# Kernel tuning notes

Hardware: AMD Instinct MI355X
Metric: run time of the kernel (lower is better)

The kernel has to match this reference:

```python
import jax, jax.numpy as jnp
import numpy as np

EMBED_DIM = 1024
NUM_HEADS = 16
HEAD_DIM = EMBED_DIM // NUM_HEADS
MAX_DIST = 128
NUM_BUCKETS = 2 * MAX_DIST + 1  # 257: fixes off-by-one in original Embedding sizing


def setup_inputs() -> dict:
    key = jax.random.key(0)
    ks = jax.random.split(key, 10)
    B, S, D = 2, 2048, EMBED_DIM
    s = 1.0 / np.sqrt(D)
    return {
        "x": jax.random.normal(ks[0], (B, S, D), dtype=jnp.float32),
        "Wq": jax.random.normal(ks[1], (D, D), dtype=jnp.float32) * s,
        "bq": jnp.zeros((D,), dtype=jnp.float32),
        "Wk": jax.random.normal(ks[2], (D, D), dtype=jnp.float32) * s,
        "bk": jnp.zeros((D,), dtype=jnp.float32),
        "Wv": jax.random.normal(ks[3], (D, D), dtype=jnp.float32) * s,
        "bv": jnp.zeros((D,), dtype=jnp.float32),
        "Wo": jax.random.normal(ks[4], (D, D), dtype=jnp.float32) * s,
        "bo": jnp.zeros((D,), dtype=jnp.float32),
        "rel_emb": jax.random.normal(ks[5], (NUM_BUCKETS, NUM_HEADS), dtype=jnp.float32) * 0.02,
    }


def _rel_bias(rel_emb, seq_len):
    # relative position clamped to [-MAX_DIST, MAX_DIST], shifted to [0, 2*MAX_DIST]
    pos = jnp.arange(seq_len)
    rel = jnp.clip(pos[:, None] - pos[None, :], -MAX_DIST, MAX_DIST) + MAX_DIST
    bias = rel_emb[rel]                    # [S, S, H]
    return jnp.transpose(bias, (2, 0, 1))  # [H, S, S]


def reference(x, Wq, bq, Wk, bk, Wv, bv, Wo, bo, rel_emb):
    B, S, D = x.shape
    H, Hd = NUM_HEADS, HEAD_DIM
    # torch Linear: y = x @ W.T + b
    q = (x @ Wq.T + bq).reshape(B, S, H, Hd).transpose(0, 2, 1, 3)  # [B,H,S,Hd]
    k = (x @ Wk.T + bk).reshape(B, S, H, Hd).transpose(0, 2, 1, 3)
    v = (x @ Wv.T + bv).reshape(B, S, H, Hd).transpose(0, 2, 1, 3)
    scores = jnp.einsum("bhqd,bhkd->bhqk", q, k) / jnp.sqrt(jnp.float32(Hd))
    scores = scores + _rel_bias(rel_emb, S)[None]  # add [H,S,S] bias
    probs = jax.nn.softmax(scores, axis=-1)
    out = jnp.einsum("bhqk,bhkd->bhqd", probs, v)
    out = out.transpose(0, 2, 1, 3).reshape(B, S, D)
    return out @ Wo.T + bo
```

## Files before the change

### kernel.cpp

```cpp
#include <hip/hip_runtime.h>
#include <hip/hip_bf16.h>
#include <cstdint>
#include <cstddef>

#define DEVI __device__ __forceinline__

static constexpr int SEQ = 2048;
static constexpr int DM  = 1024;
static constexpr int NH  = 16;
static constexpr int HD  = 64;
static constexpr int NTOK = 2 * SEQ;
static constexpr int NBUCKET = 257;
static constexpr float LOG2E = 1.44269504088896f;

typedef __attribute__((ext_vector_type(8))) short bf16x8;
typedef __attribute__((ext_vector_type(4))) float f32x4;
typedef __attribute__((ext_vector_type(16))) float f32x16;
typedef __attribute__((ext_vector_type(2))) unsigned int uint32x2;
#define MFMA16(a, b, c) __builtin_amdgcn_mfma_f32_16x16x32_bf16((a), (b), (c), 0, 0, 0)
#define MFMA32(a, b, c) __builtin_amdgcn_mfma_f32_32x32x16_bf16((a), (b), (c), 0, 0, 0)

DEVI float bf1(uint16_t u)  { return __uint_as_float(((uint32_t)u) << 16); }
DEVI uint16_t f2bf(float f) {
    uint32_t x = __float_as_uint(f);
    x += 0x7fffu + ((x >> 16) & 1u);
    return (uint16_t)(x >> 16);
}
DEVI bf16x8 ld_frag(const uint16_t* p) {
    union { uint4 u; bf16x8 f; } c;
    c.u = *(const uint4*)p;
    return c.f;
}
DEVI void gld16(const uint16_t* g, uint16_t* l) {
    __builtin_amdgcn_global_load_lds(
        (const __attribute__((address_space(1))) uint32_t*)g,
        (__attribute__((address_space(3))) uint32_t*)l, 16, 0, 0);
}
DEVI uint32_t cvt_pk_bf16(float lo, float hi) {
    uint32_t r;
    asm("v_cvt_pk_bf16_f32 %0, %1, %2" : "=v"(r) : "v"(lo), "v"(hi));
    return r;
}
DEVI void pl32(uint32_t &a, uint32_t &b) {
    const uint32x2 r = __builtin_amdgcn_permlane32_swap(a, b, false, false);
    a = r[0]; b = r[1];
}

__global__ void sniff_kernel(const uint16_t* __restrict__ x, int* __restrict__ flag)
{
    int bad = 0;
    for (int i = threadIdx.x; i < 512; i += 64) {
        const float v = bf1(x[i]);
        if (!(fabsf(v) < 64.0f)) bad = 1;
    }
    const unsigned long long m = __ballot(bad);
    if (threadIdx.x == 0) *flag = (m != 0ull) ? 1 : 0;
}

__global__ __launch_bounds__(256)
void convert_kernel(const void* __restrict__ x, const void* __restrict__ Wq,
                    const void* __restrict__ Wk, const void* __restrict__ Wv,
                    const void* __restrict__ Wo, const void* __restrict__ bq,
                    const void* __restrict__ bk, const void* __restrict__ bv,
                    const void* __restrict__ bo, uint16_t* __restrict__ dst,
                    const int* __restrict__ flagp)
{
    const bool f32in = (*flagp != 0);
    const size_t M4 = 4194304, M1 = 1048576;
    const size_t e = ((size_t)blockIdx.x * 256 + threadIdx.x) * 8;
    const void* src; size_t off;
    if      (e < M4)                 { src = x;  off = e; }
    else if (e < M4 + M1)            { src = Wq; off = e - M4; }
    else if (e < M4 + 2*M1)          { src = Wk; off = e - M4 - M1; }
    else if (e < M4 + 3*M1)          { src = Wv; off = e - M4 - 2*M1; }
    else if (e < M4 + 4*M1)          { src = Wo; off = e - M4 - 3*M1; }
    else if (e < M4 + 4*M1 + 1024)   { src = bq; off = e - M4 - 4*M1; }
    else if (e < M4 + 4*M1 + 2048)   { src = bk; off = e - M4 - 4*M1 - 1024; }
    else if (e < M4 + 4*M1 + 3072)   { src = bv; off = e - M4 - 4*M1 - 2048; }
    else                             { src = bo; off = e - M4 - 4*M1 - 3072; }
    if (f32in) {
        const float4 a = *(const float4*)((const float*)src + off);
        const float4 b = *(const float4*)((const float*)src + off + 4);
        uint4 o;
        o.x = (uint32_t)f2bf(a.x) | ((uint32_t)f2bf(a.y) << 16);
        o.y = (uint32_t)f2bf(a.z) | ((uint32_t)f2bf(a.w) << 16);
        o.z = (uint32_t)f2bf(b.x) | ((uint32_t)f2bf(b.y) << 16);
        o.w = (uint32_t)f2bf(b.z) | ((uint32_t)f2bf(b.w) << 16);
        *(uint4*)(dst + e) = o;
    } else {
        *(uint4*)(dst + e) = *(const uint4*)((const uint16_t*)src + off);
    }
}

#define QKV_STEP(AS, BS)                                                       \
  do {                                                                         \
    bf16x8 af[4], bfr[4];                                                      \
    _Pragma("unroll")                                                          \
    for (int t4 = 0; t4 < 4; ++t4) {                                           \
        af[t4]  = ld_frag(&(AS)[(wm + t4 * 16 + ln) * 32 + quad * 8]);         \
        bfr[t4] = ld_frag(&(BS)[(wn + t4 * 16 + ln) * 32 + quad * 8]);         \
    }                                                                          \
    _Pragma("unroll")                                                          \
    for (int ti = 0; ti < 4; ++ti)                                             \
      _Pragma("unroll")                                                        \
      for (int tj = 0; tj < 4; ++tj)                                           \
        acc[ti][tj] = MFMA16(af[ti], bfr[tj], acc[ti][tj]);                    \
  } while (0)

__global__ __launch_bounds__(256)
void gemm_qkv(const uint16_t* __restrict__ xc, const uint16_t* __restrict__ Wqkv,
              const uint16_t* __restrict__ bqkv,
              uint16_t* __restrict__ Qw, uint16_t* __restrict__ Kw,
              uint16_t* __restrict__ Vt)
{
    __shared__ uint16_t As[2][128 * 32];
    __shared__ uint16_t Bs[2][128 * 32];
    const int tid = threadIdx.x, bx = blockIdx.x;
    const int lane = tid & 63, wave = tid >> 6;
    const int ln = lane & 15, quad = lane >> 4;
    const int wm = (wave & 1) * 64, wn = (wave >> 1) * 64;

    const uint16_t *Ab, *Bb;
    int bm, bn, vor;
    if (bx < 512) {
        vor = 0; bm = (bx >> 4) * 128; bn = (bx & 15) * 128;
        Ab = xc + (size_t)bm * DM;  Bb = Wqkv + (size_t)bn * DM;
    } else {
        vor = 1; const int b2 = bx - 512; bm = (b2 >> 5) * 128; bn = (b2 & 31) * 128;
        Ab = Wqkv + (size_t)(2048 + bm) * DM;  Bb = xc + (size_t)bn * DM;
    }

    f32x4 acc[4][4];
    #pragma unroll
    for (int i = 0; i < 4; ++i)
        #pragma unroll
        for (int j = 0; j < 4; ++j) acc[i][j] = (f32x4){0.f, 0.f, 0.f, 0.f};

    const int s0 = tid, s1 = 256 + tid;
    const uint16_t* ga0 = Ab + (size_t)(s0 >> 2) * DM + (s0 & 3) * 8;
    const uint16_t* ga1 = Ab + (size_t)(s1 >> 2) * DM + (s1 & 3) * 8;
    const uint16_t* gb0 = Bb + (size_t)(s0 >> 2) * DM + (s0 & 3) * 8;
    const uint16_t* gb1 = Bb + (size_t)(s1 >> 2) * DM + (s1 & 3) * 8;

    gld16(ga0, &As[0][s0 * 8]);
    gld16(ga1, &As[0][s1 * 8]);
    gld16(gb0, &Bs[0][s0 * 8]);
    gld16(gb1, &Bs[0][s1 * 8]);
    __syncthreads();

    for (int t = 0; t < 16; ++t) {
        const int kB = t * 64 + 32;
        gld16(ga0 + kB, &As[1][s0 * 8]);
        gld16(ga1 + kB, &As[1][s1 * 8]);
        gld16(gb0 + kB, &Bs[1][s0 * 8]);
        gld16(gb1 + kB, &Bs[1][s1 * 8]);
        QKV_STEP(As[0], Bs[0]);
        __syncthreads();

        if (t < 15) {
            const int kA = t * 64 + 64;
            gld16(ga0 + kA, &As[0][s0 * 8]);
            gld16(ga1 + kA, &As[0][s1 * 8]);
            gld16(gb0 + kA, &Bs[0][s0 * 8]);
            gld16(gb1 + kA, &Bs[0][s1 * 8]);
        }
        QKV_STEP(As[1], Bs[1]);
        __syncthreads();
    }

    if (!vor) {
        #pragma unroll
        for (int tj = 0; tj < 4; ++tj) {
            const int c = bn + wn + tj * 16 + ln;
            const int mat = c >> 10, h = (c >> 6) & 15, hd = c & 63;
            uint16_t* dstp = mat ? Kw : Qw;
            const float scale = mat ? 1.0f : (0.125f * LOG2E);
            const float bb = bf1(bqkv[c]);
            #pragma unroll
            for (int ti = 0; ti < 4; ++ti)
                #pragma unroll
                for (int r = 0; r < 4; ++r) {
                    const int row = bm + wm + ti * 16 + quad * 4 + r;
                    const int b = row >> 11, s = row & 2047;
                    dstp[(((size_t)b * NH + h) * SEQ + s) * HD + hd] =
                        f2bf((acc[ti][tj][r] + bb) * scale);
                }
        }
    } else {
        #pragma unroll
        for (int ti = 0; ti < 4; ++ti)
            #pragma unroll
            for (int r = 0; r < 4; ++r) {
                const int f = bm + wm + ti * 16 + quad * 4 + r;
                const int h = f >> 6, hd = f & 63;
                const float bb = bf1(bqkv[2048 + f]);
                #pragma unroll
                for (int tj = 0; tj < 4; ++tj) {
                    const int t = bn + wn + tj * 16 + ln;
                    const int b = t >> 11, s = t & 2047;
                    Vt[(((size_t)b * NH + h) * HD + hd) * SEQ + s] = f2bf(acc[ti][tj][r] + bb);
                }
            }
    }
}

#define GO_STEP(AS, BS)                                                        \
  do {                                                                         \
    bf16x8 af[4], bfr[2];                                                      \
    _Pragma("unroll")                                                          \
    for (int t4 = 0; t4 < 4; ++t4)                                             \
        af[t4] = ld_frag(&(AS)[(wm + t4 * 16 + ln) * 32 + quad * 8]);          \
    _Pragma("unroll")                                                          \
    for (int t2 = 0; t2 < 2; ++t2)                                             \
        bfr[t2] = ld_frag(&(BS)[(wn + t2 * 16 + ln) * 32 + quad * 8]);         \
    _Pragma("unroll")                                                          \
    for (int ti = 0; ti < 4; ++ti)                                             \
      _Pragma("unroll")                                                        \
      for (int tj = 0; tj < 2; ++tj)                                           \
        acc[ti][tj] = MFMA16(af[ti], bfr[tj], acc[ti][tj]);                    \
  } while (0)

__global__ __launch_bounds__(256)
void gemm_out(const uint16_t* __restrict__ Cw, const uint16_t* __restrict__ Woc,
              const uint16_t* __restrict__ boc, void* __restrict__ out,
              const int* __restrict__ flagp)
{
    __shared__ uint16_t As[2][128 * 32];
    __shared__ uint16_t Bs[2][64 * 32];
    const int tid = threadIdx.x, bx = blockIdx.x;
    const int lane = tid & 63, wave = tid >> 6;
    const int ln = lane & 15, quad = lane >> 4;
    const int wm = (wave & 1) * 64, wn = (wave >> 1) * 32;
    const int bm = (bx >> 4) * 128, bn = (bx & 15) * 64;
    const uint16_t* Ab = Cw + (size_t)bm * DM;
    const uint16_t* Bb = Woc + (size_t)bn * DM;

    f32x4 acc[4][2];
    #pragma unroll
    for (int i = 0; i < 4; ++i)
        #pragma unroll
        for (int j = 0; j < 2; ++j) acc[i][j] = (f32x4){0.f, 0.f, 0.f, 0.f};

    const int s0 = tid, s1 = 256 + tid;
    const uint16_t* ga0 = Ab + (size_t)(s0 >> 2) * DM + (s0 & 3) * 8;
    const uint16_t* ga1 = Ab + (size_t)(s1 >> 2) * DM + (s1 & 3) * 8;
    const uint16_t* gb0 = Bb + (size_t)(s0 >> 2) * DM + (s0 & 3) * 8;

    gld16(ga0, &As[0][s0 * 8]);
    gld16(ga1, &As[0][s1 * 8]);
    gld16(gb0, &Bs[0][s0 * 8]);
    __syncthreads();

    for (int t = 0; t < 16; ++t) {
        const int kB = t * 64 + 32;
        gld16(ga0 + kB, &As[1][s0 * 8]);
        gld16(ga1 + kB, &As[1][s1 * 8]);
        gld16(gb0 + kB, &Bs[1][s0 * 8]);
        GO_STEP(As[0], Bs[0]);
        __syncthreads();

        if (t < 15) {
            const int kA = t * 64 + 64;
            gld16(ga0 + kA, &As[0][s0 * 8]);
            gld16(ga1 + kA, &As[0][s1 * 8]);
            gld16(gb0 + kA, &Bs[0][s0 * 8]);
        }
        GO_STEP(As[1], Bs[1]);
        __syncthreads();
    }

    const bool f32o = (*flagp != 0);
    #pragma unroll
    for (int tj = 0; tj < 2; ++tj) {
        const int c = bn + wn + tj * 16 + ln;
        const float bb = bf1(boc[c]);
        #pragma unroll
        for (int ti = 0; ti < 4; ++ti)
            #pragma unroll
            for (int r = 0; r < 4; ++r) {
                const int row = bm + wm + ti * 16 + quad * 4 + r;
                const float v = acc[ti][tj][r] + bb;
                if (f32o) ((float*)out)[(size_t)row * DM + c] = v;
                else      ((uint16_t*)out)[(size_t)row * DM + c] = f2bf(v);
            }
    }
}

#define P_BUILD(SA, PA_LO, PA_HI)                                              \
  do {                                                                         \
    uint32_t c0_ = cvt_pk_bf16((SA)[0], (SA)[1]);                              \
    uint32_t c1_ = cvt_pk_bf16((SA)[2], (SA)[3]);                              \
    uint32_t c2_ = cvt_pk_bf16((SA)[4], (SA)[5]);                              \
    uint32_t c3_ = cvt_pk_bf16((SA)[6], (SA)[7]);                              \
    uint32_t c4_ = cvt_pk_bf16((SA)[8], (SA)[9]);                              \
    uint32_t c5_ = cvt_pk_bf16((SA)[10], (SA)[11]);                            \
    uint32_t c6_ = cvt_pk_bf16((SA)[12], (SA)[13]);                            \
    uint32_t c7_ = cvt_pk_bf16((SA)[14], (SA)[15]);                            \
    pl32(c0_, c2_); pl32(c1_, c3_);                                            \
    pl32(c4_, c6_); pl32(c5_, c7_);                                            \
    union { uint32_t u[4]; bf16x8 f; } lo_, hi_;                               \
    lo_.u[0] = c0_; lo_.u[1] = c1_; lo_.u[2] = c2_; lo_.u[3] = c3_;            \
    hi_.u[0] = c4_; hi_.u[1] = c5_; hi_.u[2] = c6_; hi_.u[3] = c7_;            \
    (PA_LO) = lo_.f; (PA_HI) = hi_.f;                                          \
  } while (0)

#define ATTN_COMPUTE(K0, KSB, VSB)                                             \
  do {                                                                         \
    const int mode_ = ((K0) >= q0 + 256) ? 0 : (((K0) + 192 <= q0) ? 2 : 1);   \
    bf16x8 kf_[2][4], vf_[2][4];                                               \
    _Pragma("unroll")                                                          \
    for (int kb = 0; kb < 2; ++kb)                                             \
      _Pragma("unroll")                                                        \
      for (int ds = 0; ds < 4; ++ds)                                           \
        kf_[kb][ds] = ld_frag((KSB) + kfo[kb][ds]);                            \
    _Pragma("unroll")                                                          \
    for (int db = 0; db < 2; ++db)                                             \
      _Pragma("unroll")                                                        \
      for (int kc = 0; kc < 4; ++kc)                                           \
        vf_[db][kc] = ld_frag((VSB) + vfo[db][kc]);                            \
    f32x16 sa0, sa1;                                                           \
    {                                                                          \
      const float binit_ = (mode_ == 0) ? bneg : ((mode_ == 2) ? bpos : 0.f);  \
      _Pragma("unroll")                                                        \
      for (int r = 0; r < 16; ++r) { sa0[r] = binit_; sa1[r] = binit_; }       \
    }                                                                          \
    _Pragma("unroll")                                                          \
    for (int ds = 0; ds < 4; ++ds) {                                           \
      sa0 = MFMA32(kf_[0][ds], qb[ds], sa0);                                   \
      sa1 = MFMA32(kf_[1][ds], qb[ds], sa1);                                   \
    }                                                                          \
    if (mode_ == 1) {                                                          \
      const int iq0_ = q0 + wave * 32 + l31 + 128 - (K0) - 4 * hi;             \
      _Pragma("unroll")                                                        \
      for (int r = 0; r < 16; ++r) {                                           \
        const int ko_ = (r & 3) + 8 * (r >> 2);                                \
        const int x0_ = max(0, min(256, iq0_ - ko_));                          \
        const int x1_ = max(0, min(256, iq0_ - 32 - ko_));                     \
        sa0[r] += bias_s[x0_];                                                 \
        sa1[r] += bias_s[x1_];                                                 \
      }                                                                        \
    }                                                                          \
    _Pragma("unroll")                                                          \
    for (int r = 0; r < 16; ++r) {                                             \
      sa0[r] = __builtin_amdgcn_exp2f(sa0[r]);                                 \
      sa1[r] = __builtin_amdgcn_exp2f(sa1[r]);                                 \
    }                                                                          \
    bf16x8 pa_[4];                                                             \
    P_BUILD(sa0, pa_[0], pa_[1]);                                              \
    P_BUILD(sa1, pa_[2], pa_[3]);                                              \
    _Pragma("unroll")                                                          \
    for (int kc = 0; kc < 4; ++kc) {                                           \
      lf    = MFMA32(pa_[kc], onef, lf);                                       \
      o2[0] = MFMA32(pa_[kc], vf_[0][kc], o2[0]);                              \
      o2[1] = MFMA32(pa_[kc], vf_[1][kc], o2[1]);                              \
    }                                                                          \
  } while (0)

__global__ __launch_bounds__(256, 2)
void attn_mfma(const uint16_t* __restrict__ Q, const uint16_t* __restrict__ K,
               const uint16_t* __restrict__ Vt, const void* __restrict__ rel,
               uint16_t* __restrict__ ctx, const int* __restrict__ flagp)
{
    __shared__ alignas(16) uint16_t Ks[2][64 * 64];
    __shared__ alignas(16) uint16_t Vls[2][64 * 64];
    __shared__ float bias_s[NBUCKET];

    const bool f32in = (*flagp != 0);
    const int tid = threadIdx.x, wave = tid >> 6, lane = tid & 63;
    const int l31 = lane & 31, hi = lane >> 5;

    const int blk = blockIdx.x;
    const int bh = (blk & 7) * 4 + ((blk >> 3) & 3);
    const int qt = blk >> 5;
    const int b = bh >> 4, h = bh & 15;
    const int q0 = qt * 128;

    const float C8 = 8.0f * LOG2E;
    for (int i = tid; i < NBUCKET; i += 256) {
        const float bv = f32in ? ((const float*)rel)[i * NH + h]
                               : bf1(((const uint16_t*)rel)[i * NH + h]);
        bias_s[i] = bv * LOG2E - C8;
    }

    bf16x8 qb[4];
    {
        const uint16_t* qp = Q + ((size_t)bh * SEQ + q0 + wave * 32 + l31) * HD;
        #pragma unroll
        for (int ds = 0; ds < 4; ++ds)
            qb[ds] = ld_frag(qp + ds * 16 + hi * 8);
    }

    union { uint4 u; bf16x8 f; } onec;
    onec.u = (uint4){0x3F803F80u, 0x3F803F80u, 0x3F803F80u, 0x3F803F80u};
    const bf16x8 onef = onec.f;

    f32x16 o2[2], lf;
    #pragma unroll
    for (int r = 0; r < 16; ++r) { o2[0][r] = 0.f; o2[1][r] = 0.f; lf[r] = 0.f; }

    const int s0_ = tid, s1_ = tid + 256;
    const int r0_ = s0_ >> 3, c0s_ = (s0_ & 7) ^ (r0_ & 7);
    const int r1_ = s1_ >> 3, c1s_ = (s1_ & 7) ^ (r1_ & 7);
    const int koff0 = r0_ * HD + c0s_ * 8,  koff1 = r1_ * HD + c1s_ * 8;
    const int voff0 = r0_ * SEQ + c0s_ * 8, voff1 = r1_ * SEQ + c1s_ * 8;
    uint16_t* const kd00 = &Ks[0][s0_ * 8];
    uint16_t* const kd01 = &Ks[0][s1_ * 8];
    uint16_t* const kd10 = &Ks[1][s0_ * 8];
    uint16_t* const kd11 = &Ks[1][s1_ * 8];
    uint16_t* const vd00 = &Vls[0][s0_ * 8];
    uint16_t* const vd01 = &Vls[0][s1_ * 8];
    uint16_t* const vd10 = &Vls[1][s0_ * 8];
    uint16_t* const vd11 = &Vls[1][s1_ * 8];

    const uint16_t* kg = K  + (size_t)bh * SEQ * HD;
    const uint16_t* vg = Vt + (size_t)bh * HD * SEQ;

    const int swz = l31 & 7;
    int kfo[2][4], vfo[2][4];
    #pragma unroll
    for (int kb = 0; kb < 2; ++kb)
        #pragma unroll
        for (int ds = 0; ds < 4; ++ds)
            kfo[kb][ds] = (kb * 32 + l31) * 64 + ((ds * 2 + hi) ^ swz) * 8;
    #pragma unroll
    for (int db = 0; db < 2; ++db)
        #pragma unroll
        for (int kc = 0; kc < 4; ++kc)
            vfo[db][kc] = (db * 32 + l31) * 64 + ((kc * 2 + hi) ^ swz) * 8;

    gld16(kg + koff0, kd00); gld16(kg + koff1, kd01);
    gld16(vg + voff0, vd00); gld16(vg + voff1, vd01);
    kg += 64 * HD; vg += 64;
    __syncthreads();
    const float bneg = bias_s[0], bpos = bias_s[256];

    for (int t = 0; t < 16; ++t) {
        gld16(kg + koff0, kd10); gld16(kg + koff1, kd11);
        gld16(vg + voff0, vd10); gld16(vg + voff1, vd11);
        kg += 64 * HD; vg += 64;
        ATTN_COMPUTE(t * 128, &Ks[0][0], &Vls[0][0]);
        __syncthreads();

        if (t < 15) {
            gld16(kg + koff0, kd00); gld16(kg + koff1, kd01);
            gld16(vg + voff0, vd00); gld16(vg + voff1, vd01);
            kg += 64 * HD; vg += 64;
        }
        ATTN_COMPUTE(t * 128 + 64, &Ks[1][0], &Vls[1][0]);
        __syncthreads();
    }

    #pragma unroll
    for (int r = 0; r < 16; ++r) {
        const float inv = 1.0f / lf[r];
        const int qq = q0 + wave * 32 + (r & 3) + 8 * (r >> 2) + 4 * hi;
        #pragma unroll
        for (int db = 0; db < 2; ++db)
            ctx[(((size_t)b * SEQ + qq) * NH + h) * HD + db * 32 + l31] =
                f2bf(o2[db][r] * inv);
    }
}

extern "C" void kernel_launch(void* const* d_in, const int* in_sizes, int n_in,
                              void* d_out, int out_size, void* d_ws, size_t ws_size,
                              hipStream_t stream)
{
    const void* x   = d_in[0];
    const void* Wq  = d_in[1];
    const void* bq  = d_in[2];
    const void* Wk  = d_in[3];
    const void* bk  = d_in[4];
    const void* Wv  = d_in[5];
    const void* bv  = d_in[6];
    const void* Wo  = d_in[7];
    const void* bo  = d_in[8];
    const void* rel = d_in[9];

    const size_t M4 = 4194304, M1 = 1048576;
    uint16_t* ws16 = (uint16_t*)d_ws;
    uint16_t* xc   = ws16;
    uint16_t* Wqkv = ws16 + M4;
    uint16_t* Woc  = ws16 + M4 + 3 * M1;
    uint16_t* bqkv = ws16 + M4 + 4 * M1;
    uint16_t* boc  = bqkv + 3072;
    uint16_t* Qw   = ws16 + M4 + 4 * M1 + 8192;
    uint16_t* Kw   = Qw + M4;
    uint16_t* Vt   = Kw + M4;
    int* flag = (int*)(Vt + M4);
    uint16_t* Cw = xc;

    sniff_kernel<<<1, 64, 0, stream>>>((const uint16_t*)x, flag);
    convert_kernel<<<4098, 256, 0, stream>>>(x, Wq, Wk, Wv, Wo, bq, bk, bv, bo,
                                             ws16, flag);
    gemm_qkv<<<768, 256, 0, stream>>>(xc, Wqkv, bqkv, Qw, Kw, Vt);
    attn_mfma<<<512, 256, 0, stream>>>(Qw, Kw, Vt, rel, Cw, flag);
    gemm_out<<<512, 256, 0, stream>>>(Cw, Woc, boc, d_out, flag);
}
```

Measured before the change: 207.9 us.

## Fold dtype sniff into convert kernel and double-buffer 128-key attention stages

After: 205.8 us. Within noise of the previous version (-1.0%).

```diff
diff --git a/kernel.cpp b/kernel.cpp
--- a/kernel.cpp
+++ b/kernel.cpp
@@ -46,26 +46,27 @@
     a = r[0]; b = r[1];
 }
 
-__global__ void sniff_kernel(const uint16_t* __restrict__ x, int* __restrict__ flag)
-{
-    int bad = 0;
-    for (int i = threadIdx.x; i < 512; i += 64) {
-        const float v = bf1(x[i]);
-        if (!(fabsf(v) < 64.0f)) bad = 1;
-    }
-    const unsigned long long m = __ballot(bad);
-    if (threadIdx.x == 0) *flag = (m != 0ull) ? 1 : 0;
-}
-
 __global__ __launch_bounds__(256)
 void convert_kernel(const void* __restrict__ x, const void* __restrict__ Wq,
                     const void* __restrict__ Wk, const void* __restrict__ Wv,
                     const void* __restrict__ Wo, const void* __restrict__ bq,
                     const void* __restrict__ bk, const void* __restrict__ bv,
                     const void* __restrict__ bo, uint16_t* __restrict__ dst,
-                    const int* __restrict__ flagp)
+                    int* __restrict__ flag_out)
 {
-    const bool f32in = (*flagp != 0);
+    __shared__ int f32s;
+    if (threadIdx.x == 0) f32s = 0;
+    __syncthreads();
+    int bad = 0;
+    for (int i = threadIdx.x; i < 512; i += 256) {
+        const float v = bf1(((const uint16_t*)x)[i]);
+        if (!(fabsf(v) < 64.0f)) bad = 1;
+    }
+    if (bad) f32s = 1;
+    __syncthreads();
+    const bool f32in = (f32s != 0);
+    if (blockIdx.x == 0 && threadIdx.x == 0) *flag_out = f32in ? 1 : 0;
+
     const size_t M4 = 4194304, M1 = 1048576;
     const size_t e = ((size_t)blockIdx.x * 256 + threadIdx.x) * 8;
     const void* src; size_t off;
@@ -356,13 +357,21 @@
     }                                                                          \
   } while (0)
 
+#define STAGE_T(p, st, n)                                                      \
+  do {                                                                         \
+    gld16(Kb  + (size_t)(n) * 64 * HD + koff0, &Ks[p][st][s0_ * 8]);           \
+    gld16(Kb  + (size_t)(n) * 64 * HD + koff1, &Ks[p][st][s1_ * 8]);           \
+    gld16(Vtb + (n) * 64 + voff0,              &Vls[p][st][s0_ * 8]);          \
+    gld16(Vtb + (n) * 64 + voff1,              &Vls[p][st][s1_ * 8]);          \
+  } while (0)
+
 __global__ __launch_bounds__(256, 2)
 void attn_mfma(const uint16_t* __restrict__ Q, const uint16_t* __restrict__ K,
                const uint16_t* __restrict__ Vt, const void* __restrict__ rel,
                uint16_t* __restrict__ ctx, const int* __restrict__ flagp)
 {
-    __shared__ alignas(16) uint16_t Ks[2][64 * 64];
-    __shared__ alignas(16) uint16_t Vls[2][64 * 64];
+    __shared__ alignas(16) uint16_t Ks[2][2][4096];
+    __shared__ alignas(16) uint16_t Vls[2][2][4096];
     __shared__ float bias_s[NBUCKET];
 
     const bool f32in = (*flagp != 0);
@@ -403,17 +412,9 @@
     const int r1_ = s1_ >> 3, c1s_ = (s1_ & 7) ^ (r1_ & 7);
     const int koff0 = r0_ * HD + c0s_ * 8,  koff1 = r1_ * HD + c1s_ * 8;
     const int voff0 = r0_ * SEQ + c0s_ * 8, voff1 = r1_ * SEQ + c1s_ * 8;
-    uint16_t* const kd00 = &Ks[0][s0_ * 8];
-    uint16_t* const kd01 = &Ks[0][s1_ * 8];
-    uint16_t* const kd10 = &Ks[1][s0_ * 8];
-    uint16_t* const kd11 = &Ks[1][s1_ * 8];
-    uint16_t* const vd00 = &Vls[0][s0_ * 8];
-    uint16_t* const vd01 = &Vls[0][s1_ * 8];
-    uint16_t* const vd10 = &Vls[1][s0_ * 8];
-    uint16_t* const vd11 = &Vls[1][s1_ * 8];
-
-    const uint16_t* kg = K  + (size_t)bh * SEQ * HD;
-    const uint16_t* vg = Vt + (size_t)bh * HD * SEQ;
+
+    const uint16_t* Kb  = K  + (size_t)bh * SEQ * HD;
+    const uint16_t* Vtb = Vt + (size_t)bh * HD * SEQ;
 
     const int swz = l31 & 7;
     int kfo[2][4], vfo[2][4];
@@ -428,25 +429,19 @@
         for (int kc = 0; kc < 4; ++kc)
             vfo[db][kc] = (db * 32 + l31) * 64 + ((kc * 2 + hi) ^ swz) * 8;
 
-    gld16(kg + koff0, kd00); gld16(kg + koff1, kd01);
-    gld16(vg + voff0, vd00); gld16(vg + voff1, vd01);
-    kg += 64 * HD; vg += 64;
+    STAGE_T(0, 0, 0);
+    STAGE_T(0, 1, 1);
     __syncthreads();
     const float bneg = bias_s[0], bpos = bias_s[256];
 
     for (int t = 0; t < 16; ++t) {
-        gld16(kg + koff0, kd10); gld16(kg + koff1, kd11);
-        gld16(vg + voff0, vd10); gld16(vg + voff1, vd11);
-        kg += 64 * HD; vg += 64;
-        ATTN_COMPUTE(t * 128, &Ks[0][0], &Vls[0][0]);
-        __syncthreads();
-
+        const int p = t & 1, np = p ^ 1;
         if (t < 15) {
-            gld16(kg + koff0, kd00); gld16(kg + koff1, kd01);
-            gld16(vg + voff0, vd00); gld16(vg + voff1, vd01);
-            kg += 64 * HD; vg += 64;
+            STAGE_T(np, 0, 2 * t + 2);
+            STAGE_T(np, 1, 2 * t + 3);
         }
-        ATTN_COMPUTE(t * 128 + 64, &Ks[1][0], &Vls[1][0]);
+        ATTN_COMPUTE(t * 128,      &Ks[p][0][0], &Vls[p][0][0]);
+        ATTN_COMPUTE(t * 128 + 64, &Ks[p][1][0], &Vls[p][1][0]);
         __syncthreads();
     }
 
@@ -489,7 +484,6 @@
     int* flag = (int*)(Vt + M4);
     uint16_t* Cw = xc;
 
-    sniff_kernel<<<1, 64, 0, stream>>>((const uint16_t*)x, flag);
     convert_kernel<<<4098, 256, 0, stream>>>(x, Wq, Wk, Wv, Wo, bq, bk, bv, bo,
                                              ws16, flag);
     gemm_qkv<<<768, 256, 0, stream>>>(xc, Wqkv, bqkv, Qw, Kw, Vt);
```
